# Optimization experiments

Hardware: AMD Instinct MI355X
Metric: run time of the kernel (lower is better)

Reference implementation:

```python
import jax, jax.numpy as jnp
import numpy as np

N_HEADS = 16
HEAD_SIZE = 64
SEQ_LEN = 2048
EMBED = 1024
BATCH = 2


def setup_inputs() -> dict:
    key = jax.random.key(0)
    ks = jax.random.split(key, 9)
    d_inner = N_HEADS * HEAD_SIZE
    s = 1.0 / np.sqrt(EMBED)
    inp = {
        "inputs": jax.random.normal(ks[0], (BATCH, SEQ_LEN, EMBED), jnp.float32),
        "Wq": jax.random.uniform(ks[1], (EMBED, d_inner), jnp.float32, -s, s),
        "bq": jax.random.uniform(ks[2], (d_inner,), jnp.float32, -s, s),
        "Wk": jax.random.uniform(ks[3], (EMBED, d_inner), jnp.float32, -s, s),
        "bk": jax.random.uniform(ks[4], (d_inner,), jnp.float32, -s, s),
        "Wv": jax.random.uniform(ks[5], (EMBED, d_inner), jnp.float32, -s, s),
        "bv": jax.random.uniform(ks[6], (d_inner,), jnp.float32, -s, s),
        "Wo": jax.random.uniform(ks[7], (d_inner, EMBED), jnp.float32, -s, s),
        "bo": jax.random.uniform(ks[8], (EMBED,), jnp.float32, -s, s),
    }
    return inp


def reference(inputs, Wq, bq, Wk, bk, Wv, bv, Wo, bo):
    B, S, _ = inputs.shape
    # QKV projections -> [B, H, S, Dh]
    def proj(W, b):
        return (inputs @ W + b).reshape(B, S, N_HEADS, HEAD_SIZE).transpose(0, 2, 1, 3)
    q, k, v = proj(Wq, bq), proj(Wk, bk), proj(Wv, bv)
    scores = jnp.einsum("bhqd,bhkd->bhqk", q, k) / jnp.sqrt(jnp.float32(HEAD_SIZE))
    causal = jnp.tril(jnp.ones((S, S), dtype=bool))  # [S, S]
    scores = jnp.where(causal[None, None], scores, -jnp.inf)
    attn = jax.nn.softmax(scores, axis=-1)  # dropout is identity in eval
    out = jnp.einsum("bhqk,bhkd->bhqd", attn, v)
    out = out.transpose(0, 2, 1, 3).reshape(B, S, N_HEADS * HEAD_SIZE)
    return out @ Wo + bo
```

## Files before the change

### kernel.cpp

```cpp
#include <hip/hip_runtime.h>
#include <hip/hip_bf16.h>
#include <math.h>

#define NH 16
#define DH 64
#define SEQ 2048
#define EMBED 1024
#define DINNER 1024
#define BATCH 2
#define MTOK 4096

typedef __bf16 bf16x8 __attribute__((ext_vector_type(8)));
typedef float  f32x4  __attribute__((ext_vector_type(4)));
typedef float  f32x16 __attribute__((ext_vector_type(16)));
typedef unsigned int u32;

__device__ __forceinline__ void gload16(const void* g, void* l) {
    __builtin_amdgcn_global_load_lds((const __attribute__((address_space(1))) void*)g,
                                     (__attribute__((address_space(3))) void*)l, 16, 0, 0);
}

__global__ __launch_bounds__(256) void cvt_bf16(
    const float* __restrict__ src, __bf16* __restrict__ dst, int n)
{
    int i = (blockIdx.x * 256 + threadIdx.x) * 4;
    if (i + 3 < n) {
        float4 v = *(const float4*)&src[i];
        dst[i + 0] = (__bf16)v.x;
        dst[i + 1] = (__bf16)v.y;
        dst[i + 2] = (__bf16)v.z;
        dst[i + 3] = (__bf16)v.w;
    }
}

__global__ __launch_bounds__(256) void tconv4(
    const float* __restrict__ W0, const float* __restrict__ W1,
    const float* __restrict__ W2, const float* __restrict__ W3,
    __bf16* __restrict__ D0, __bf16* __restrict__ D1,
    __bf16* __restrict__ D2, __bf16* __restrict__ D3)
{
    const int z = blockIdx.z;
    const float* __restrict__ src = (z == 0) ? W0 : (z == 1) ? W1 : (z == 2) ? W2 : W3;
    __bf16* __restrict__ dst      = (z == 0) ? D0 : (z == 1) ? D1 : (z == 2) ? D2 : D3;
    const int R = 1024, C = 1024;

    __shared__ float t[32][33];
    const int c0 = blockIdx.x * 32, r0 = blockIdx.y * 32;
    const int x = threadIdx.x & 31, y = threadIdx.x >> 5;
#pragma unroll
    for (int i = 0; i < 4; ++i)
        t[y + 8 * i][x] = src[(size_t)(r0 + y + 8 * i) * C + c0 + x];
    __syncthreads();
#pragma unroll
    for (int i = 0; i < 4; ++i)
        dst[(size_t)(c0 + y + 8 * i) * R + r0 + x] = (__bf16)t[x][y + 8 * i];
}

#define QSCALE 0.18033688f

__global__ __launch_bounds__(256) void gemm128(
    const __bf16* __restrict__ A,
    const __bf16* __restrict__ Bt0, const __bf16* __restrict__ Bt1, const __bf16* __restrict__ Bt2,
    const float* __restrict__ b0, const float* __restrict__ b1, const float* __restrict__ b2,
    void* __restrict__ o0, void* __restrict__ o1, void* __restrict__ o2,
    int Kdim, int mode3)
{
    const int z = blockIdx.z;
    const __bf16* __restrict__ Bt = (z == 0) ? Bt0 : (z == 1) ? Bt1 : Bt2;
    const float*  __restrict__ bias = (z == 0) ? b0 : (z == 1) ? b1 : b2;
    void* __restrict__ outp = (z == 0) ? o0 : (z == 1) ? o1 : o2;
    const int mode = mode3 ? 3 : z;
    const float scale = (mode == 0) ? QSCALE : 1.0f;

    __shared__ __bf16 As[128 * 32];
    __shared__ __bf16 Bs[128 * 32];

    const int tid  = threadIdx.x;
    const int lane = tid & 63;
    const int wid  = tid >> 6;
    const int wm = wid >> 1, wn = wid & 1;
    const int ls = lane & 15, lg = lane >> 4;
    const int m0 = blockIdx.y * 128, n0 = blockIdx.x * 128;

    const int sr = tid >> 2;
    const int sc = (tid & 3) * 8;

    f32x4 acc[4][4] = {};

    for (int k0 = 0; k0 < Kdim; k0 += 32) {
        gload16(&A [(size_t)(m0 + sr)      * Kdim + k0 + sc], &As[sr * 32 + sc]);
        gload16(&A [(size_t)(m0 + 64 + sr) * Kdim + k0 + sc], &As[(64 + sr) * 32 + sc]);
        gload16(&Bt[(size_t)(n0 + sr)      * Kdim + k0 + sc], &Bs[sr * 32 + sc]);
        gload16(&Bt[(size_t)(n0 + 64 + sr) * Kdim + k0 + sc], &Bs[(64 + sr) * 32 + sc]);
        __syncthreads();

        bf16x8 af[4], bfr[4];
#pragma unroll
        for (int i = 0; i < 4; ++i) {
            af[i]  = *(const bf16x8*)&As[(wm * 64 + i * 16 + ls) * 32 + lg * 8];
            bfr[i] = *(const bf16x8*)&Bs[(wn * 64 + i * 16 + ls) * 32 + lg * 8];
        }
#pragma unroll
        for (int i = 0; i < 4; ++i)
#pragma unroll
            for (int jx = 0; jx < 4; ++jx)
                acc[i][jx] = __builtin_amdgcn_mfma_f32_16x16x32_bf16(af[i], bfr[jx], acc[i][jx], 0, 0, 0);
        __syncthreads();
    }

#pragma unroll
    for (int i = 0; i < 4; ++i) {
#pragma unroll
        for (int jx = 0; jx < 4; ++jx) {
#pragma unroll
            for (int j = 0; j < 4; ++j) {
                const int m = m0 + wm * 64 + i * 16 + lg * 4 + j;
                const int n = n0 + wn * 64 + jx * 16 + ls;
                const float v = (acc[i][jx][j] + bias[n]) * scale;
                if (mode == 3) {
                    ((float*)outp)[(size_t)m * EMBED + n] = v;
                } else {
                    const int b = m >> 11, s = m & 2047;
                    const int h = n >> 6,  d = n & 63;
                    if (mode == 2)
                        ((__bf16*)outp)[(((size_t)(b * NH + h) * DH + d) << 11) + s] = (__bf16)v;
                    else
                        ((__bf16*)outp)[((((size_t)(b * NH + h) << 11) + s) * DH) + d] = (__bf16)v;
                }
            }
        }
    }
}

__global__ __launch_bounds__(64) void attn_mfma(
    const __bf16* __restrict__ Q, const __bf16* __restrict__ K,
    const __bf16* __restrict__ Vt, __bf16* __restrict__ ctx)
{
    __shared__ __bf16 lds[8192];

    const int lane = threadIdx.x & 63;
    const int col  = lane & 31;
    const int hi   = lane >> 5;
    const int bh   = blockIdx.x & 31;
    const int qt32 = 63 - (blockIdx.x >> 5);
    const int qlo  = qt32 * 32;
    const int b = bh >> 4, h = bh & 15;

    const __bf16* __restrict__ Qb = Q + ((size_t)bh << 11) * DH;
    const char* __restrict__ Kg = (const char*)(K  + ((size_t)bh << 11) * DH);
    const char* __restrict__ Vg = (const char*)(Vt + ((size_t)bh << 11) * DH);

    char* ldsK = (char*)&lds[0];
    char* ldsV = ldsK + 8192;

    const int srow = lane >> 3;
    const int sswz = ((lane & 7) * 16) ^ (srow << 4);
    const int swz  = (col & 7) << 4;

    bf16x8 qf[4];
#pragma unroll
    for (int c = 0; c < 4; ++c)
        qf[c] = *(const bf16x8*)&Qb[(size_t)(qlo + col) * DH + c * 16 + hi * 8];

    const int nt = (qt32 + 2) >> 1;

#pragma unroll
    for (int i = 0; i < 8; ++i)
        gload16(Kg + (size_t)(i * 8 + srow) * 128 + sswz, ldsK + i * 1024 + lane * 16);
#pragma unroll
    for (int i = 0; i < 8; ++i)
        gload16(Vg + (size_t)(i * 8 + srow) * 4096 + sswz, ldsV + i * 1024 + lane * 16);

    f32x16 oT0 = {}, oT1 = {};
    float mrun = -INFINITY, lrun = 0.f;

    for (int t = 0; t < nt; ++t) {
        const int k0 = t * 64;

        asm volatile("s_waitcnt vmcnt(8)" ::: "memory");

        bf16x8 kfa[4], kfb[4];
#pragma unroll
        for (int c = 0; c < 4; ++c) {
            kfa[c] = *(const bf16x8*)(ldsK + (     col) * 128 + ((c * 32 + hi * 16) ^ swz));
            kfb[c] = *(const bf16x8*)(ldsK + (32 + col) * 128 + ((c * 32 + hi * 16) ^ swz));
        }

        __builtin_amdgcn_s_setprio(1);
        f32x16 sta = {}, stb = {};
#pragma unroll
        for (int c = 0; c < 4; ++c) {
            sta = __builtin_amdgcn_mfma_f32_32x32x16_bf16(kfa[c], qf[c], sta, 0, 0, 0);
            stb = __builtin_amdgcn_mfma_f32_32x32x16_bf16(kfb[c], qf[c], stb, 0, 0, 0);
        }
        __builtin_amdgcn_s_setprio(0);

        asm volatile("s_waitcnt lgkmcnt(0)" ::: "memory");
        __builtin_amdgcn_sched_barrier(0);
        if (t + 1 < nt) {
            const int kbn = (t + 1) * 64;
#pragma unroll
            for (int i = 0; i < 8; ++i)
                gload16(Kg + (size_t)(kbn + i * 8 + srow) * 128 + sswz,
                        ldsK + i * 1024 + lane * 16);
        }

        if (k0 + 63 > qlo) {
#pragma unroll
            for (int r = 0; r < 16; ++r) {
                const int krel = (r & 3) + 8 * (r >> 2) + 4 * hi;
                if (k0 + krel > qlo + col)      sta[r] = -INFINITY;
                if (k0 + 32 + krel > qlo + col) stb[r] = -INFINITY;
            }
        }

        float ta = fmaxf(fmaxf(fmaxf(sta[0], sta[1]), fmaxf(sta[2], sta[3])),
                         fmaxf(fmaxf(sta[4], sta[5]), fmaxf(sta[6], sta[7])));
        float tb = fmaxf(fmaxf(fmaxf(sta[8], sta[9]),  fmaxf(sta[10], sta[11])),
                         fmaxf(fmaxf(sta[12], sta[13]), fmaxf(sta[14], sta[15])));
        float tc = fmaxf(fmaxf(fmaxf(stb[0], stb[1]), fmaxf(stb[2], stb[3])),
                         fmaxf(fmaxf(stb[4], stb[5]), fmaxf(stb[6], stb[7])));
        float td = fmaxf(fmaxf(fmaxf(stb[8], stb[9]),  fmaxf(stb[10], stb[11])),
                         fmaxf(fmaxf(stb[12], stb[13]), fmaxf(stb[14], stb[15])));
        float tmax = fmaxf(fmaxf(ta, tb), fmaxf(tc, td));
        tmax = fmaxf(tmax, __shfl_xor(tmax, 32));

        if (__any(tmax > mrun + 8.f)) {
            const float mnew = fmaxf(mrun, tmax);
            const float corr = exp2f(mrun - mnew);
            lrun *= corr;
            oT0 *= corr;
            oT1 *= corr;
            mrun = mnew;
        }

        float pa[16], pb[16];
#pragma unroll
        for (int r = 0; r < 16; ++r) { pa[r] = exp2f(sta[r] - mrun); pb[r] = exp2f(stb[r] - mrun); }
        float psa = (((pa[0] + pa[1]) + (pa[2] + pa[3])) + ((pa[4] + pa[5]) + (pa[6] + pa[7])))
                  + (((pa[8] + pa[9]) + (pa[10] + pa[11])) + ((pa[12] + pa[13]) + (pa[14] + pa[15])));
        float psb = (((pb[0] + pb[1]) + (pb[2] + pb[3])) + ((pb[4] + pb[5]) + (pb[6] + pb[7])))
                  + (((pb[8] + pb[9]) + (pb[10] + pb[11])) + ((pb[12] + pb[13]) + (pb[14] + pb[15])));
        float psum = psa + psb;
        psum += __shfl_xor(psum, 32);
        lrun += psum;

        u32 wa[8], wb[8];
#pragma unroll
        for (int i = 0; i < 8; ++i) {
            u32 r1, r2;
            asm("v_cvt_pk_bf16_f32 %0, %1, %2" : "=v"(r1) : "v"(pa[2 * i]), "v"(pa[2 * i + 1]));
            asm("v_cvt_pk_bf16_f32 %0, %1, %2" : "=v"(r2) : "v"(pb[2 * i]), "v"(pb[2 * i + 1]));
            wa[i] = r1; wb[i] = r2;
        }
        asm("v_permlane32_swap_b32 %0, %1" : "+v"(wa[0]), "+v"(wa[2]));
        asm("v_permlane32_swap_b32 %0, %1" : "+v"(wa[1]), "+v"(wa[3]));
        asm("v_permlane32_swap_b32 %0, %1" : "+v"(wa[4]), "+v"(wa[6]));
        asm("v_permlane32_swap_b32 %0, %1" : "+v"(wa[5]), "+v"(wa[7]));
        asm("v_permlane32_swap_b32 %0, %1" : "+v"(wb[0]), "+v"(wb[2]));
        asm("v_permlane32_swap_b32 %0, %1" : "+v"(wb[1]), "+v"(wb[3]));
        asm("v_permlane32_swap_b32 %0, %1" : "+v"(wb[4]), "+v"(wb[6]));
        asm("v_permlane32_swap_b32 %0, %1" : "+v"(wb[5]), "+v"(wb[7]));

        union { u32 u4[4]; bf16x8 v; } cA0, cA1, cB0, cB1;
        cA0.u4[0] = wa[0]; cA0.u4[1] = wa[1]; cA0.u4[2] = wa[2]; cA0.u4[3] = wa[3];
        cA1.u4[0] = wa[4]; cA1.u4[1] = wa[5]; cA1.u4[2] = wa[6]; cA1.u4[3] = wa[7];
        cB0.u4[0] = wb[0]; cB0.u4[1] = wb[1]; cB0.u4[2] = wb[2]; cB0.u4[3] = wb[3];
        cB1.u4[0] = wb[4]; cB1.u4[1] = wb[5]; cB1.u4[2] = wb[6]; cB1.u4[3] = wb[7];

        if (t + 1 < nt) { asm volatile("s_waitcnt vmcnt(8)" ::: "memory"); }
        else            { asm volatile("s_waitcnt vmcnt(0)" ::: "memory"); }

        __builtin_amdgcn_s_setprio(1);
#pragma unroll
        for (int dh = 0; dh < 2; ++dh) {
            bf16x8 v0 = *(const bf16x8*)(ldsV + (dh * 32 + col) * 128 + ((0  + hi * 16) ^ swz));
            bf16x8 v1 = *(const bf16x8*)(ldsV + (dh * 32 + col) * 128 + ((32 + hi * 16) ^ swz));
            bf16x8 v2 = *(const bf16x8*)(ldsV + (dh * 32 + col) * 128 + ((64 + hi * 16) ^ swz));
            bf16x8 v3 = *(const bf16x8*)(ldsV + (dh * 32 + col) * 128 + ((96 + hi * 16) ^ swz));
            f32x16& o = dh ? oT1 : oT0;
            o = __builtin_amdgcn_mfma_f32_32x32x16_bf16(v0, cA0.v, o, 0, 0, 0);
            o = __builtin_amdgcn_mfma_f32_32x32x16_bf16(v1, cA1.v, o, 0, 0, 0);
            o = __builtin_amdgcn_mfma_f32_32x32x16_bf16(v2, cB0.v, o, 0, 0, 0);
            o = __builtin_amdgcn_mfma_f32_32x32x16_bf16(v3, cB1.v, o, 0, 0, 0);
        }
        __builtin_amdgcn_s_setprio(0);

        asm volatile("s_waitcnt lgkmcnt(0)" ::: "memory");
        __builtin_amdgcn_sched_barrier(0);
        if (t + 1 < nt) {
            const int kbn = (t + 1) * 64;
#pragma unroll
            for (int i = 0; i < 8; ++i)
                gload16(Vg + (size_t)(i * 8 + srow) * 4096 + (size_t)kbn * 2 + sswz,
                        ldsV + i * 1024 + lane * 16);
        }
    }

    const float inv = 1.0f / lrun;
    const size_t base = ((size_t)(b * SEQ + qlo + col)) * DINNER + h * 64;
#pragma unroll
    for (int g = 0; g < 4; ++g) {
        __bf16 t4[4];
#pragma unroll
        for (int j = 0; j < 4; ++j) t4[j] = (__bf16)(oT0[4 * g + j] * inv);
        *(uint2*)&ctx[base + 8 * g + 4 * hi] = *(uint2*)t4;
#pragma unroll
        for (int j = 0; j < 4; ++j) t4[j] = (__bf16)(oT1[4 * g + j] * inv);
        *(uint2*)&ctx[base + 32 + 8 * g + 4 * hi] = *(uint2*)t4;
    }
}

extern "C" void kernel_launch(void* const* d_in, const int* in_sizes, int n_in,
                              void* d_out, int out_size, void* d_ws, size_t ws_size,
                              hipStream_t stream)
{
    const float* X  = (const float*)d_in[0];
    const float* Wq = (const float*)d_in[1];
    const float* bq = (const float*)d_in[2];
    const float* Wk = (const float*)d_in[3];
    const float* bk = (const float*)d_in[4];
    const float* Wv = (const float*)d_in[5];
    const float* bv = (const float*)d_in[6];
    const float* Wo = (const float*)d_in[7];
    const float* bo = (const float*)d_in[8];
    float* out = (float*)d_out;

    __bf16* ws  = (__bf16*)d_ws;
    const size_t MI = 1048576;
    __bf16* Xb   = ws;
    __bf16* Wtq  = ws + 4  * MI;
    __bf16* Wtk  = ws + 5  * MI;
    __bf16* Wtv  = ws + 6  * MI;
    __bf16* Wto  = ws + 7  * MI;
    __bf16* Qb   = ws + 8  * MI;
    __bf16* Kb   = ws + 12 * MI;
    __bf16* Vtb  = ws + 16 * MI;
    __bf16* ctxb = ws + 20 * MI;

    cvt_bf16<<<dim3(MTOK * EMBED / 1024), dim3(256), 0, stream>>>(X, Xb, MTOK * EMBED);
    tconv4<<<dim3(32, 32, 4), dim3(256), 0, stream>>>(Wq, Wk, Wv, Wo, Wtq, Wtk, Wtv, Wto);

    {
        dim3 grid(DINNER / 128, MTOK / 128, 3), blk(256);
        gemm128<<<grid, blk, 0, stream>>>(Xb, Wtq, Wtk, Wtv, bq, bk, bv,
                                          Qb, Kb, Vtb, EMBED, 0);
    }

    {
        dim3 grid(32 * (SEQ / 32)), blk(64);
        attn_mfma<<<grid, blk, 0, stream>>>(Qb, Kb, Vtb, ctxb);
    }

    {
        dim3 grid(EMBED / 128, MTOK / 128, 1), blk(256);
        gemm128<<<grid, blk, 0, stream>>>(ctxb, Wto, Wto, Wto, bo, bo, bo,
                                          out, out, out, DINNER, 1);
    }
}
```

Before: 145.3 us.

## Split KV loop for long causal query tiles and merge partials

Query tiles in the upper half of the sequence now run their KV loop in two interleaved halves on separate blocks. Each half writes a normalized partial output plus its running max and sum, and a new merge kernel combines them with log-sum-exp weights. This is meant to even out per-block work under the causal mask and raise parallelism in the attention kernel. In exchange it adds an extra kernel launch, reuses freed workspace buffers for partials, and adds extra global traffic plus a bf16 rounding of the partial outputs.

```diff
diff --git a/kernel.cpp b/kernel.cpp
--- a/kernel.cpp
+++ b/kernel.cpp
@@ -134,16 +134,34 @@
 
 __global__ __launch_bounds__(64) void attn_mfma(
     const __bf16* __restrict__ Q, const __bf16* __restrict__ K,
-    const __bf16* __restrict__ Vt, __bf16* __restrict__ ctx)
+    const __bf16* __restrict__ Vt, __bf16* __restrict__ ctx,
+    __bf16* __restrict__ Opart, float* __restrict__ ml)
 {
     __shared__ __bf16 lds[8192];
 
     const int lane = threadIdx.x & 63;
     const int col  = lane & 31;
     const int hi   = lane >> 5;
-    const int bh   = blockIdx.x & 31;
-    const int qt32 = 63 - (blockIdx.x >> 5);
-    const int qlo  = qt32 * 32;
+    const int bi   = blockIdx.x;
+
+    int bh, qt32, tstart, tstep;
+    bool split;
+    if (bi < 2048) {
+        const int sh = bi >> 5;
+        qt32 = 63 - (sh >> 1);
+        tstart = sh & 1;
+        tstep = 2;
+        bh = bi & 31;
+        split = true;
+    } else {
+        const int j = bi - 2048;
+        qt32 = 31 - (j >> 5);
+        tstart = 0;
+        tstep = 1;
+        bh = j & 31;
+        split = false;
+    }
+    const int qlo = qt32 * 32;
     const int b = bh >> 4, h = bh & 15;
 
     const __bf16* __restrict__ Qb = Q + ((size_t)bh << 11) * DH;
@@ -164,17 +182,21 @@
 
     const int nt = (qt32 + 2) >> 1;
 
-#pragma unroll
-    for (int i = 0; i < 8; ++i)
-        gload16(Kg + (size_t)(i * 8 + srow) * 128 + sswz, ldsK + i * 1024 + lane * 16);
-#pragma unroll
-    for (int i = 0; i < 8; ++i)
-        gload16(Vg + (size_t)(i * 8 + srow) * 4096 + sswz, ldsV + i * 1024 + lane * 16);
+    {
+        const int kp0 = tstart * 64;
+#pragma unroll
+        for (int i = 0; i < 8; ++i)
+            gload16(Kg + (size_t)(kp0 + i * 8 + srow) * 128 + sswz, ldsK + i * 1024 + lane * 16);
+#pragma unroll
+        for (int i = 0; i < 8; ++i)
+            gload16(Vg + (size_t)(i * 8 + srow) * 4096 + (size_t)kp0 * 2 + sswz,
+                    ldsV + i * 1024 + lane * 16);
+    }
 
     f32x16 oT0 = {}, oT1 = {};
     float mrun = -INFINITY, lrun = 0.f;
 
-    for (int t = 0; t < nt; ++t) {
+    for (int t = tstart; t < nt; t += tstep) {
         const int k0 = t * 64;
 
         asm volatile("s_waitcnt vmcnt(8)" ::: "memory");
@@ -197,8 +219,8 @@
 
         asm volatile("s_waitcnt lgkmcnt(0)" ::: "memory");
         __builtin_amdgcn_sched_barrier(0);
-        if (t + 1 < nt) {
-            const int kbn = (t + 1) * 64;
+        if (t + tstep < nt) {
+            const int kbn = (t + tstep) * 64;
 #pragma unroll
             for (int i = 0; i < 8; ++i)
                 gload16(Kg + (size_t)(kbn + i * 8 + srow) * 128 + sswz,
@@ -268,8 +290,8 @@
         cB0.u4[0] = wb[0]; cB0.u4[1] = wb[1]; cB0.u4[2] = wb[2]; cB0.u4[3] = wb[3];
         cB1.u4[0] = wb[4]; cB1.u4[1] = wb[5]; cB1.u4[2] = wb[6]; cB1.u4[3] = wb[7];
 
-        if (t + 1 < nt) { asm volatile("s_waitcnt vmcnt(8)" ::: "memory"); }
-        else            { asm volatile("s_waitcnt vmcnt(0)" ::: "memory"); }
+        if (t + tstep < nt) { asm volatile("s_waitcnt vmcnt(8)" ::: "memory"); }
+        else                { asm volatile("s_waitcnt vmcnt(0)" ::: "memory"); }
 
         __builtin_amdgcn_s_setprio(1);
 #pragma unroll
@@ -288,8 +310,8 @@
 
         asm volatile("s_waitcnt lgkmcnt(0)" ::: "memory");
         __builtin_amdgcn_sched_barrier(0);
-        if (t + 1 < nt) {
-            const int kbn = (t + 1) * 64;
+        if (t + tstep < nt) {
+            const int kbn = (t + tstep) * 64;
 #pragma unroll
             for (int i = 0; i < 8; ++i)
                 gload16(Vg + (size_t)(i * 8 + srow) * 4096 + (size_t)kbn * 2 + sswz,
@@ -298,16 +320,62 @@
     }
 
     const float inv = 1.0f / lrun;
-    const size_t base = ((size_t)(b * SEQ + qlo + col)) * DINNER + h * 64;
-#pragma unroll
-    for (int g = 0; g < 4; ++g) {
-        __bf16 t4[4];
-#pragma unroll
-        for (int j = 0; j < 4; ++j) t4[j] = (__bf16)(oT0[4 * g + j] * inv);
-        *(uint2*)&ctx[base + 8 * g + 4 * hi] = *(uint2*)t4;
-#pragma unroll
-        for (int j = 0; j < 4; ++j) t4[j] = (__bf16)(oT1[4 * g + j] * inv);
-        *(uint2*)&ctx[base + 32 + 8 * g + 4 * hi] = *(uint2*)t4;
+    if (!split) {
+        const size_t base = ((size_t)(b * SEQ + qlo + col)) * DINNER + h * 64;
+#pragma unroll
+        for (int g = 0; g < 4; ++g) {
+            __bf16 t4[4];
+#pragma unroll
+            for (int j = 0; j < 4; ++j) t4[j] = (__bf16)(oT0[4 * g + j] * inv);
+            *(uint2*)&ctx[base + 8 * g + 4 * hi] = *(uint2*)t4;
+#pragma unroll
+            for (int j = 0; j < 4; ++j) t4[j] = (__bf16)(oT1[4 * g + j] * inv);
+            *(uint2*)&ctx[base + 32 + 8 * g + 4 * hi] = *(uint2*)t4;
+        }
+    } else {
+        const size_t pbase = (size_t)bi * 2048 + col * 64;
+#pragma unroll
+        for (int g = 0; g < 4; ++g) {
+            __bf16 t4[4];
+#pragma unroll
+            for (int j = 0; j < 4; ++j) t4[j] = (__bf16)(oT0[4 * g + j] * inv);
+            *(uint2*)&Opart[pbase + 8 * g + 4 * hi] = *(uint2*)t4;
+#pragma unroll
+            for (int j = 0; j < 4; ++j) t4[j] = (__bf16)(oT1[4 * g + j] * inv);
+            *(uint2*)&Opart[pbase + 32 + 8 * g + 4 * hi] = *(uint2*)t4;
+        }
+        if (hi == 0) {
+            ml[(size_t)bi * 64 + col]      = mrun;
+            ml[(size_t)bi * 64 + 32 + col] = lrun;
+        }
+    }
+}
+
+__global__ __launch_bounds__(64) void attn_merge(
+    const __bf16* __restrict__ Opart, const float* __restrict__ ml,
+    __bf16* __restrict__ ctx)
+{
+    const int lane = threadIdx.x & 63;
+    const int mk = blockIdx.x;
+    const int qt32 = 32 + (mk >> 5);
+    const int bh = mk & 31;
+    const int b = bh >> 4, h = bh & 15;
+    const int su0 = (63 - qt32) * 64 + bh;
+    const int su1 = su0 + 32;
+
+    for (int r = 0; r < 32; ++r) {
+        const float m0 = ml[(size_t)su0 * 64 + r];
+        const float l0 = ml[(size_t)su0 * 64 + 32 + r];
+        const float m1 = ml[(size_t)su1 * 64 + r];
+        const float l1 = ml[(size_t)su1 * 64 + 32 + r];
+        const float M  = fmaxf(m0, m1);
+        const float w0 = l0 * exp2f(m0 - M);
+        const float w1 = l1 * exp2f(m1 - M);
+        const float inv = 1.0f / (w0 + w1);
+        const float o0 = (float)Opart[(size_t)su0 * 2048 + r * 64 + lane];
+        const float o1 = (float)Opart[(size_t)su1 * 2048 + r * 64 + lane];
+        ctx[((size_t)(b * SEQ + qt32 * 32 + r)) * DINNER + h * 64 + lane] =
+            (__bf16)((o0 * w0 + o1 * w1) * inv);
     }
 }
 
@@ -337,6 +405,8 @@
     __bf16* Kb   = ws + 12 * MI;
     __bf16* Vtb  = ws + 16 * MI;
     __bf16* ctxb = ws + 20 * MI;
+    __bf16* Opart = Xb;
+    float*  mlbuf = (float*)(ws + 4 * MI);
 
     cvt_bf16<<<dim3(MTOK * EMBED / 1024), dim3(256), 0, stream>>>(X, Xb, MTOK * EMBED);
     tconv4<<<dim3(32, 32, 4), dim3(256), 0, stream>>>(Wq, Wk, Wv, Wo, Wtq, Wtk, Wtv, Wto);
@@ -348,8 +418,10 @@
     }
 
     {
-        dim3 grid(32 * (SEQ / 32)), blk(64);
-        attn_mfma<<<grid, blk, 0, stream>>>(Qb, Kb, Vtb, ctxb);
+        dim3 grid(3072), blk(64);
+        attn_mfma<<<grid, blk, 0, stream>>>(Qb, Kb, Vtb, ctxb, Opart, mlbuf);
+        dim3 grid2(1024), blk2(64);
+        attn_merge<<<grid2, blk2, 0, stream>>>(Opart, mlbuf, ctxb);
     }
 
     {
```

New measurement: 156.7 us, median of 2. 7.8% more time.
